# Optimization experiments

Measured on AMD Instinct MI355X. Metric: run time of the kernel, lower is better.

## Reference

```python
import jax, jax.numpy as jnp
import numpy as np

N_NODES = 50000
N_EDGES = 600000
N_GRAPHS = 64
IN_C, HID_C, OUT_C = 128, 128, 64


def gcn_conv(x, edge_index, W, b, num_nodes):
    """PyG GCNConv: x' = D^-1/2 (A + I) D^-1/2 (x W) + b, messages src->dst."""
    src, dst = edge_index[0], edge_index[1]
    # add self-loops
    loop = jnp.arange(num_nodes, dtype=src.dtype)
    src_full = jnp.concatenate([src, loop])
    dst_full = jnp.concatenate([dst, loop])
    # degree of A+I counted at the aggregation (dst) side
    deg = jax.ops.segment_sum(jnp.ones_like(dst_full, dtype=x.dtype), dst_full,
                              num_segments=num_nodes)
    dinv = jax.lax.rsqrt(jnp.maximum(deg, 1.0))
    norm = dinv[src_full] * dinv[dst_full]              # [E+N]
    h = x @ W                                           # [N, C_out] dense GEMM
    msg = h[src_full] * norm[:, None]                   # gather + scale
    out = jax.ops.segment_sum(msg, dst_full, num_segments=num_nodes)  # scatter-add
    return out + b


def global_mean_pool(x, batch, num_graphs):
    s = jax.ops.segment_sum(x, batch, num_segments=num_graphs)
    cnt = jax.ops.segment_sum(jnp.ones_like(batch, dtype=x.dtype), batch,
                              num_segments=num_graphs)
    return s / jnp.maximum(cnt, 1.0)[:, None]


def setup_inputs() -> dict:
    key = jax.random.key(0)
    ks = jax.random.split(key, 8)
    x = jax.random.normal(ks[0], (N_NODES, IN_C), dtype=jnp.float32)
    edge_index = jax.random.randint(ks[1], (2, N_EDGES), 0, N_NODES, dtype=jnp.int64)
    batch = jnp.sort(jax.random.randint(ks[2], (N_NODES,), 0, N_GRAPHS, dtype=jnp.int64))
    # Glorot-style init like PyG defaults
    W1 = jax.random.normal(ks[3], (IN_C, HID_C), dtype=jnp.float32) * (1.0 / np.sqrt(IN_C))
    b1 = jnp.zeros((HID_C,), dtype=jnp.float32)
    W2 = jax.random.normal(ks[4], (HID_C, OUT_C), dtype=jnp.float32) * (1.0 / np.sqrt(HID_C))
    b2 = jnp.zeros((OUT_C,), dtype=jnp.float32)
    return {"x": x, "W1": W1, "b1": b1, "W2": W2, "b2": b2,
            "edge_index": edge_index, "batch": batch}


def reference(x, W1, b1, W2, b2, edge_index, batch):
    h = gcn_conv(x, edge_index, W1, b1, N_NODES)
    h = jax.nn.relu(h)
    h = gcn_conv(h, edge_index, W2, b2, N_NODES)
    return global_mean_pool(h, batch, N_GRAPHS)  # [N_GRAPHS, OUT_C]
```

## Files before the change

kernel.cpp:

```cpp
#include <hip/hip_runtime.h>

#define NN 50000
#define NE 600000
#define NG 64
#define SCAN_T 1024
#define SCAN_NB ((NN + SCAN_T - 1) / SCAN_T)
#define PSPLIT 16

typedef unsigned int uint_t;
typedef unsigned short ushort_t;
typedef __attribute__((ext_vector_type(8))) short bf16x8;
typedef __attribute__((ext_vector_type(4))) float f32x4;

__device__ __forceinline__ ushort_t f2bf(float x) {
    uint_t u = __builtin_bit_cast(uint_t, x);
    u = (u + 0x7FFFu + ((u >> 16) & 1u)) >> 16;
    return (ushort_t)u;
}
__device__ __forceinline__ float bf_lo(uint_t p) {
    uint_t v = p << 16; return __builtin_bit_cast(float, v);
}
__device__ __forceinline__ float bf_hi(uint_t p) {
    uint_t v = p & 0xFFFF0000u; return __builtin_bit_cast(float, v);
}

__global__ void k_zero_deg(int* __restrict__ deg) {
    int i = blockIdx.x * blockDim.x + threadIdx.x;
    if (i < NN) deg[i] = 0;
}

__global__ void k_hist(const int* __restrict__ dst, int* __restrict__ deg) {
    int e = blockIdx.x * blockDim.x + threadIdx.x;
    if (e < NE) atomicAdd(&deg[dst[e]], 1);
}

__global__ __launch_bounds__(SCAN_T) void k_scan1(const int* __restrict__ deg,
                                                  int* __restrict__ blockSums) {
    __shared__ int s[SCAN_T];
    int i = blockIdx.x * SCAN_T + threadIdx.x;
    s[threadIdx.x] = (i < NN) ? deg[i] : 0;
    __syncthreads();
    for (int off = SCAN_T / 2; off > 0; off >>= 1) {
        if (threadIdx.x < off) s[threadIdx.x] += s[threadIdx.x + off];
        __syncthreads();
    }
    if (threadIdx.x == 0) blockSums[blockIdx.x] = s[0];
}

__global__ void k_scan2(const int* __restrict__ blockSums, int* __restrict__ blockOffs) {
    int t = threadIdx.x;
    int orig = (t < SCAN_NB) ? blockSums[t] : 0;
    int v = orig;
    for (int off = 1; off < 64; off <<= 1) {
        int u = __shfl_up(v, off);
        if (t >= off) v += u;
    }
    if (t < SCAN_NB) blockOffs[t] = v - orig;
}

__global__ __launch_bounds__(SCAN_T) void k_scan3(const int* __restrict__ deg,
                                                  const int* __restrict__ blockOffs,
                                                  int* __restrict__ rowptr,
                                                  int* __restrict__ cursor,
                                                  float* __restrict__ dinv) {
    __shared__ int s[SCAN_T];
    const int t = threadIdx.x;
    const int i = blockIdx.x * SCAN_T + t;
    const int v = (i < NN) ? deg[i] : 0;
    s[t] = v;
    __syncthreads();
    for (int off = 1; off < SCAN_T; off <<= 1) {
        int u = (t >= off) ? s[t - off] : 0;
        int cur = s[t];
        __syncthreads();
        s[t] = cur + u;
        __syncthreads();
    }
    if (i < NN) {
        int ex = blockOffs[blockIdx.x] + s[t] - v;
        rowptr[i] = ex;
        cursor[i] = ex;
        dinv[i] = rsqrtf((float)(v + 1));
    }
    if (i == 0) rowptr[NN] = NE;
}

__global__ void k_scatter(const int* __restrict__ src, const int* __restrict__ dst,
                          int* __restrict__ cursor, int* __restrict__ csr_src) {
    int e = blockIdx.x * blockDim.x + threadIdx.x;
    if (e >= NE) return;
    int d = dst[e];
    int p = atomicAdd(&cursor[d], 1);
    csr_src[p] = src[e];
}

__global__ void k_wprep(const float* __restrict__ W, ushort_t* __restrict__ Wt) {
    int idx = blockIdx.x * 256 + threadIdx.x;
    if (idx >= 128 * 128) return;
    int k = idx >> 7, n = idx & 127;
    Wt[n * 128 + k] = f2bf(W[idx]);
}

__global__ __launch_bounds__(256) void k_gemm_mfma(const float* __restrict__ X,
                                                   const ushort_t* __restrict__ Wt,
                                                   const float* __restrict__ dinv,
                                                   ushort_t* __restrict__ Hb) {
    __shared__ ushort_t xs[128 * 128];
    __shared__ ushort_t ws[128 * 128];
    const int tid = threadIdx.x;
    const int row0 = blockIdx.x * 128;

    for (int idx = tid; idx < 128 * 32; idx += 256) {
        int r = idx >> 5, c4 = idx & 31;
        int row = row0 + r;
        float4 v = make_float4(0.f, 0.f, 0.f, 0.f);
        if (row < NN) v = ((const float4*)X)[(long)row * 32 + c4];
        ushort4 o;
        o.x = f2bf(v.x); o.y = f2bf(v.y); o.z = f2bf(v.z); o.w = f2bf(v.w);
        uint_t byte = (uint_t)(r * 256 + c4 * 8) ^ (uint_t)((r & 7) << 4);
        *(ushort4*)((char*)xs + byte) = o;
    }
    for (int idx = tid; idx < 128 * 16; idx += 256) {
        int n = idx >> 4, c16 = idx & 15;
        uint4 v = ((const uint4*)Wt)[idx];
        uint_t byte = (uint_t)(n * 256 + c16 * 16) ^ (uint_t)((n & 7) << 4);
        *(uint4*)((char*)ws + byte) = v;
    }
    __syncthreads();

    const int w = tid >> 6;
    const int l = tid & 63;
    const int m0 = (w >> 1) * 4;
    const int n0 = (w & 1) * 4;
    const int lr = l & 15;
    const int kg = l >> 4;

    f32x4 acc[4][4] = {};
    for (int kk = 0; kk < 4; ++kk) {
        const int kb = kk * 64 + kg * 16;
        bf16x8 a[4], b[4];
#pragma unroll
        for (int m = 0; m < 4; ++m) {
            int r = (m0 + m) * 16 + lr;
            uint_t byte = (uint_t)(r * 256 + kb) ^ (uint_t)((r & 7) << 4);
            a[m] = *(const bf16x8*)((const char*)xs + byte);
        }
#pragma unroll
        for (int n = 0; n < 4; ++n) {
            int r = (n0 + n) * 16 + lr;
            uint_t byte = (uint_t)(r * 256 + kb) ^ (uint_t)((r & 7) << 4);
            b[n] = *(const bf16x8*)((const char*)ws + byte);
        }
#pragma unroll
        for (int m = 0; m < 4; ++m)
#pragma unroll
            for (int n = 0; n < 4; ++n)
                acc[m][n] = __builtin_amdgcn_mfma_f32_16x16x32_bf16(a[m], b[n], acc[m][n], 0, 0, 0);
    }

#pragma unroll
    for (int m = 0; m < 4; ++m) {
#pragma unroll
        for (int r = 0; r < 4; ++r) {
            int row = row0 + (m0 + m) * 16 + kg * 4 + r;
            if (row < NN) {
                float sc = dinv[row];
#pragma unroll
                for (int n = 0; n < 4; ++n) {
                    int col = (n0 + n) * 16 + lr;
                    Hb[(long)row * 128 + col] = f2bf(acc[m][n][r] * sc);
                }
            }
        }
    }
}

template <int C, int EPI>
__global__ __launch_bounds__(256) void k_agg(const int* __restrict__ rowptr,
                                             const int* __restrict__ csr_src,
                                             const float* __restrict__ dinv,
                                             const ushort_t* __restrict__ Hb,
                                             const float* __restrict__ bias,
                                             void* __restrict__ OUT) {
    constexpr int TPN = C / 8;
    constexpr int NPB = 256 / TPN;
    const int node = blockIdx.x * NPB + threadIdx.x / TPN;
    if (node >= NN) return;
    const int lane = threadIdx.x % TPN;
    const float dd = dinv[node];
    const uint4* __restrict__ H4 = (const uint4*)Hb;

    float a0, a1, a2, a3, a4, a5, a6, a7;
    {
        uint4 sv = H4[(long)node * TPN + lane];
        a0 = bf_lo(sv.x); a1 = bf_hi(sv.x);
        a2 = bf_lo(sv.y); a3 = bf_hi(sv.y);
        a4 = bf_lo(sv.z); a5 = bf_hi(sv.z);
        a6 = bf_lo(sv.w); a7 = bf_hi(sv.w);
    }

    const int beg = rowptr[node], end = rowptr[node + 1];
    int k = beg;
    const int n4 = beg + ((end - beg) & ~3);
    for (; k < n4; k += 4) {
        int s0 = csr_src[k + 0];
        int s1 = csr_src[k + 1];
        int s2 = csr_src[k + 2];
        int s3 = csr_src[k + 3];
        uint4 h0 = H4[(long)s0 * TPN + lane];
        uint4 h1 = H4[(long)s1 * TPN + lane];
        uint4 h2 = H4[(long)s2 * TPN + lane];
        uint4 h3 = H4[(long)s3 * TPN + lane];
        a0 += (bf_lo(h0.x) + bf_lo(h1.x)) + (bf_lo(h2.x) + bf_lo(h3.x));
        a1 += (bf_hi(h0.x) + bf_hi(h1.x)) + (bf_hi(h2.x) + bf_hi(h3.x));
        a2 += (bf_lo(h0.y) + bf_lo(h1.y)) + (bf_lo(h2.y) + bf_lo(h3.y));
        a3 += (bf_hi(h0.y) + bf_hi(h1.y)) + (bf_hi(h2.y) + bf_hi(h3.y));
        a4 += (bf_lo(h0.z) + bf_lo(h1.z)) + (bf_lo(h2.z) + bf_lo(h3.z));
        a5 += (bf_hi(h0.z) + bf_hi(h1.z)) + (bf_hi(h2.z) + bf_hi(h3.z));
        a6 += (bf_lo(h0.w) + bf_lo(h1.w)) + (bf_lo(h2.w) + bf_lo(h3.w));
        a7 += (bf_hi(h0.w) + bf_hi(h1.w)) + (bf_hi(h2.w) + bf_hi(h3.w));
    }
    for (; k < end; ++k) {
        int s = csr_src[k];
        uint4 h = H4[(long)s * TPN + lane];
        a0 += bf_lo(h.x); a1 += bf_hi(h.x);
        a2 += bf_lo(h.y); a3 += bf_hi(h.y);
        a4 += bf_lo(h.z); a5 += bf_hi(h.z);
        a6 += bf_lo(h.w); a7 += bf_hi(h.w);
    }

    a0 *= dd; a1 *= dd; a2 *= dd; a3 *= dd;
    a4 *= dd; a5 *= dd; a6 *= dd; a7 *= dd;

    if (EPI == 0) {
        const float4 b0 = *(const float4*)&bias[lane * 8];
        const float4 b1 = *(const float4*)&bias[lane * 8 + 4];
        a0 = fmaxf(a0 + b0.x, 0.f) * dd; a1 = fmaxf(a1 + b0.y, 0.f) * dd;
        a2 = fmaxf(a2 + b0.z, 0.f) * dd; a3 = fmaxf(a3 + b0.w, 0.f) * dd;
        a4 = fmaxf(a4 + b1.x, 0.f) * dd; a5 = fmaxf(a5 + b1.y, 0.f) * dd;
        a6 = fmaxf(a6 + b1.z, 0.f) * dd; a7 = fmaxf(a7 + b1.w, 0.f) * dd;
    }
    uint4 o;
    o.x = (uint_t)f2bf(a0) | ((uint_t)f2bf(a1) << 16);
    o.y = (uint_t)f2bf(a2) | ((uint_t)f2bf(a3) << 16);
    o.z = (uint_t)f2bf(a4) | ((uint_t)f2bf(a5) << 16);
    o.w = (uint_t)f2bf(a6) | ((uint_t)f2bf(a7) << 16);
    ((uint4*)OUT)[(long)node * TPN + lane] = o;
}

__global__ __launch_bounds__(256) void k_pool1(const ushort_t* __restrict__ V,
                                               const int* __restrict__ batch,
                                               float* __restrict__ partial) {
    const int g = blockIdx.x / PSPLIT;
    const int s = blockIdx.x % PSPLIT;
    int beg, end;
    {
        int lo = 0, hi = NN;
        while (lo < hi) { int mid = (lo + hi) >> 1; if (batch[mid] < g) lo = mid + 1; else hi = mid; }
        beg = lo;
        lo = beg; hi = NN;
        while (lo < hi) { int mid = (lo + hi) >> 1; if (batch[mid] < g + 1) lo = mid + 1; else hi = mid; }
        end = lo;
    }
    const int c = threadIdx.x & 31;
    const int rg = threadIdx.x >> 5;
    const uint2* __restrict__ V2 = (const uint2*)V;

    float4 acc = make_float4(0.f, 0.f, 0.f, 0.f);
    for (int n = beg + s * 8 + rg; n < end; n += PSPLIT * 8) {
        uint2 h = V2[(long)n * 32 + c];
        acc.x += bf_lo(h.x); acc.y += bf_hi(h.x);
        acc.z += bf_lo(h.y); acc.w += bf_hi(h.y);
    }
    __shared__ float4 red[8][33];
    red[rg][c] = acc;
    __syncthreads();
    if (rg == 0) {
        float4 t = red[0][c];
#pragma unroll
        for (int i = 1; i < 8; ++i) {
            float4 u = red[i][c];
            t.x += u.x; t.y += u.y; t.z += u.z; t.w += u.w;
        }
        ((float4*)partial)[(long)blockIdx.x * 32 + c] = t;
    }
}

__global__ __launch_bounds__(128) void k_pool2gemm(const float* __restrict__ partial,
                                                   const int* __restrict__ batch,
                                                   const float* __restrict__ W2,
                                                   const float* __restrict__ b2,
                                                   float* __restrict__ out) {
    const int g = blockIdx.x;
    const int t = threadIdx.x;
    int beg, end;
    {
        int lo = 0, hi = NN;
        while (lo < hi) { int mid = (lo + hi) >> 1; if (batch[mid] < g) lo = mid + 1; else hi = mid; }
        beg = lo;
        lo = beg; hi = NN;
        while (lo < hi) { int mid = (lo + hi) >> 1; if (batch[mid] < g + 1) lo = mid + 1; else hi = mid; }
        end = lo;
    }
    const int cnt = end - beg;
    __shared__ float P[128];
    float s = 0.f;
    for (int i = 0; i < PSPLIT; ++i) s += partial[(long)(g * PSPLIT + i) * 128 + t];
    P[t] = (cnt > 0) ? s / (float)cnt : 0.f;
    __syncthreads();
    if (t < 64) {
        float acc = 0.f;
        for (int k = 0; k < 128; ++k) acc += P[k] * W2[k * 64 + t];
        out[g * 64 + t] = (cnt > 0) ? acc + b2[t] : 0.f;
    }
}

extern "C" void kernel_launch(void* const* d_in, const int* in_sizes, int n_in,
                              void* d_out, int out_size, void* d_ws, size_t ws_size,
                              hipStream_t stream) {
    const float* x  = (const float*)d_in[0];
    const float* W1 = (const float*)d_in[1];
    const float* b1 = (const float*)d_in[2];
    const float* W2 = (const float*)d_in[3];
    const float* b2 = (const float*)d_in[4];
    const int* ei   = (const int*)d_in[5];
    const int* src  = ei;
    const int* dst  = ei + NE;
    const int* batch = (const int*)d_in[6];
    float* out = (float*)d_out;

    char* p = (char*)d_ws;
    int* deg       = (int*)p;          p += (size_t)NN * 4;
    int* rowptr    = (int*)p;          p += (size_t)(NN + 4) * 4;
    int* cursor    = (int*)p;          p += (size_t)NN * 4;
    int* csr_src   = (int*)p;          p += (size_t)NE * 4;
    int* blockSums = (int*)p;          p += (size_t)64 * 4;
    int* blockOffs = (int*)p;          p += (size_t)64 * 4;
    float* dinv    = (float*)p;        p += (size_t)NN * 4;
    float* partial = (float*)p;        p += (size_t)NG * PSPLIT * 128 * 4;
    ushort_t* Wt   = (ushort_t*)p;     p += (size_t)128 * 128 * 2;
    ushort_t* Hb   = (ushort_t*)p;     p += (size_t)NN * 128 * 2;
    ushort_t* H1b  = (ushort_t*)p;     p += (size_t)NN * 128 * 2;
    ushort_t* Vb   = (ushort_t*)p;     p += (size_t)NN * 128 * 2;

    k_wprep<<<64, 256, 0, stream>>>(W1, Wt);
    k_zero_deg<<<(NN + 255) / 256, 256, 0, stream>>>(deg);
    k_hist<<<(NE + 255) / 256, 256, 0, stream>>>(dst, deg);
    k_scan1<<<SCAN_NB, SCAN_T, 0, stream>>>(deg, blockSums);
    k_scan2<<<1, 64, 0, stream>>>(blockSums, blockOffs);
    k_scan3<<<SCAN_NB, SCAN_T, 0, stream>>>(deg, blockOffs, rowptr, cursor, dinv);
    k_scatter<<<(NE + 255) / 256, 256, 0, stream>>>(src, dst, cursor, csr_src);

    k_gemm_mfma<<<(NN + 127) / 128, 256, 0, stream>>>(x, Wt, dinv, Hb);
    k_agg<128, 0><<<(NN + 15) / 16, 256, 0, stream>>>(rowptr, csr_src, dinv, Hb, b1, H1b);

    k_agg<128, 1><<<(NN + 15) / 16, 256, 0, stream>>>(rowptr, csr_src, dinv, H1b, b1 , Vb);

    k_pool1<<<NG * PSPLIT, 256, 0, stream>>>(Vb, batch, partial);
    k_pool2gemm<<<NG, 128, 0, stream>>>(partial, batch, W2, b2, out);
}
```

Before: 168.0 us.

## Apply second-layer weight before aggregation to shrink gather width to 64

Restores the order GEMM-then-aggregate for layer 2. A new MFMA kernel multiplies the layer-1 output by W2 (scaled by dinv) into a 64-channel buffer, so the second gather/scatter pass and the pooling move 64 channels instead of 128. It also merges the tiny block-offset scan into the third scan kernel, removing one launch. The cost is an extra GEMM launch plus writing and reading the intermediate buffer, in exchange for halving the traffic of the edge-bound aggregation.

Measured after the change: 159.1 us. -5.3%, faster.

```diff
diff --git a/kernel.cpp b/kernel.cpp
--- a/kernel.cpp
+++ b/kernel.cpp
@@ -32,6 +32,19 @@
 __global__ void k_hist(const int* __restrict__ dst, int* __restrict__ deg) {
     int e = blockIdx.x * blockDim.x + threadIdx.x;
     if (e < NE) atomicAdd(&deg[dst[e]], 1);
+}
+
+__global__ void k_wprep(const float* __restrict__ W1, const float* __restrict__ W2,
+                        ushort_t* __restrict__ W1t, ushort_t* __restrict__ W2t) {
+    int idx = blockIdx.x * 256 + threadIdx.x;
+    if (idx < 128 * 128) {
+        int k = idx >> 7, n = idx & 127;
+        W1t[n * 128 + k] = f2bf(W1[idx]);
+    } else if (idx < 128 * 128 + 128 * 64) {
+        int j = idx - 128 * 128;
+        int k = j >> 6, n = j & 63;
+        W2t[n * 128 + k] = f2bf(W2[j]);
+    }
 }
 
 __global__ __launch_bounds__(SCAN_T) void k_scan1(const int* __restrict__ deg,
@@ -47,24 +60,23 @@
     if (threadIdx.x == 0) blockSums[blockIdx.x] = s[0];
 }
 
-__global__ void k_scan2(const int* __restrict__ blockSums, int* __restrict__ blockOffs) {
-    int t = threadIdx.x;
-    int orig = (t < SCAN_NB) ? blockSums[t] : 0;
-    int v = orig;
-    for (int off = 1; off < 64; off <<= 1) {
-        int u = __shfl_up(v, off);
-        if (t >= off) v += u;
-    }
-    if (t < SCAN_NB) blockOffs[t] = v - orig;
-}
-
 __global__ __launch_bounds__(SCAN_T) void k_scan3(const int* __restrict__ deg,
-                                                  const int* __restrict__ blockOffs,
+                                                  const int* __restrict__ blockSums,
                                                   int* __restrict__ rowptr,
                                                   int* __restrict__ cursor,
                                                   float* __restrict__ dinv) {
+    __shared__ int offs[64];
     __shared__ int s[SCAN_T];
     const int t = threadIdx.x;
+    if (t < 64) {
+        int orig = (t < SCAN_NB) ? blockSums[t] : 0;
+        int v = orig;
+        for (int off = 1; off < 64; off <<= 1) {
+            int u = __shfl_up(v, off);
+            if (t >= off) v += u;
+        }
+        offs[t] = v - orig;
+    }
     const int i = blockIdx.x * SCAN_T + t;
     const int v = (i < NN) ? deg[i] : 0;
     s[t] = v;
@@ -77,7 +89,7 @@
         __syncthreads();
     }
     if (i < NN) {
-        int ex = blockOffs[blockIdx.x] + s[t] - v;
+        int ex = offs[blockIdx.x] + s[t] - v;
         rowptr[i] = ex;
         cursor[i] = ex;
         dinv[i] = rsqrtf((float)(v + 1));
@@ -92,13 +104,6 @@
     int d = dst[e];
     int p = atomicAdd(&cursor[d], 1);
     csr_src[p] = src[e];
-}
-
-__global__ void k_wprep(const float* __restrict__ W, ushort_t* __restrict__ Wt) {
-    int idx = blockIdx.x * 256 + threadIdx.x;
-    if (idx >= 128 * 128) return;
-    int k = idx >> 7, n = idx & 127;
-    Wt[n * 128 + k] = f2bf(W[idx]);
 }
 
 __global__ __launch_bounds__(256) void k_gemm_mfma(const float* __restrict__ X,
@@ -175,13 +180,84 @@
     }
 }
 
+__global__ __launch_bounds__(256) void k_gemm_mfma2(const ushort_t* __restrict__ H1,
+                                                    const ushort_t* __restrict__ W2t,
+                                                    const float* __restrict__ dinv,
+                                                    ushort_t* __restrict__ G) {
+    __shared__ ushort_t xs[128 * 128];
+    __shared__ ushort_t ws2[64 * 128];
+    const int tid = threadIdx.x;
+    const int row0 = blockIdx.x * 128;
+
+    for (int idx = tid; idx < 128 * 16; idx += 256) {
+        int r = idx >> 4, c16 = idx & 15;
+        int row = row0 + r;
+        uint4 v = make_uint4(0u, 0u, 0u, 0u);
+        if (row < NN) v = ((const uint4*)H1)[(long)row * 16 + c16];
+        uint_t byte = (uint_t)(r * 256 + c16 * 16) ^ (uint_t)((r & 7) << 4);
+        *(uint4*)((char*)xs + byte) = v;
+    }
+    for (int idx = tid; idx < 64 * 16; idx += 256) {
+        int n = idx >> 4, c16 = idx & 15;
+        uint4 v = ((const uint4*)W2t)[idx];
+        uint_t byte = (uint_t)(n * 256 + c16 * 16) ^ (uint_t)((n & 7) << 4);
+        *(uint4*)((char*)ws2 + byte) = v;
+    }
+    __syncthreads();
+
+    const int w = tid >> 6;
+    const int l = tid & 63;
+    const int lr = l & 15;
+    const int kg = l >> 4;
+    const int m0 = w * 2;
+
+    f32x4 acc[2][4] = {};
+    for (int kk = 0; kk < 4; ++kk) {
+        const int kb = kk * 64 + kg * 16;
+        bf16x8 a[2], b[4];
+#pragma unroll
+        for (int m = 0; m < 2; ++m) {
+            int r = (m0 + m) * 16 + lr;
+            uint_t byte = (uint_t)(r * 256 + kb) ^ (uint_t)((r & 7) << 4);
+            a[m] = *(const bf16x8*)((const char*)xs + byte);
+        }
+#pragma unroll
+        for (int n = 0; n < 4; ++n) {
+            int r = n * 16 + lr;
+            uint_t byte = (uint_t)(r * 256 + kb) ^ (uint_t)((r & 7) << 4);
+            b[n] = *(const bf16x8*)((const char*)ws2 + byte);
+        }
+#pragma unroll
+        for (int m = 0; m < 2; ++m)
+#pragma unroll
+            for (int n = 0; n < 4; ++n)
+                acc[m][n] = __builtin_amdgcn_mfma_f32_16x16x32_bf16(a[m], b[n], acc[m][n], 0, 0, 0);
+    }
+
+#pragma unroll
+    for (int m = 0; m < 2; ++m) {
+#pragma unroll
+        for (int r = 0; r < 4; ++r) {
+            int row = row0 + (m0 + m) * 16 + kg * 4 + r;
+            if (row < NN) {
+                float sc = dinv[row];
+#pragma unroll
+                for (int n = 0; n < 4; ++n) {
+                    int col = n * 16 + lr;
+                    G[(long)row * 64 + col] = f2bf(acc[m][n][r] * sc);
+                }
+            }
+        }
+    }
+}
+
 template <int C, int EPI>
 __global__ __launch_bounds__(256) void k_agg(const int* __restrict__ rowptr,
                                              const int* __restrict__ csr_src,
                                              const float* __restrict__ dinv,
                                              const ushort_t* __restrict__ Hb,
                                              const float* __restrict__ bias,
-                                             void* __restrict__ OUT) {
+                                             ushort_t* __restrict__ OUT) {
     constexpr int TPN = C / 8;
     constexpr int NPB = 256 / TPN;
     const int node = blockIdx.x * NPB + threadIdx.x / TPN;
@@ -235,10 +311,10 @@
     if (EPI == 0) {
         const float4 b0 = *(const float4*)&bias[lane * 8];
         const float4 b1 = *(const float4*)&bias[lane * 8 + 4];
-        a0 = fmaxf(a0 + b0.x, 0.f) * dd; a1 = fmaxf(a1 + b0.y, 0.f) * dd;
-        a2 = fmaxf(a2 + b0.z, 0.f) * dd; a3 = fmaxf(a3 + b0.w, 0.f) * dd;
-        a4 = fmaxf(a4 + b1.x, 0.f) * dd; a5 = fmaxf(a5 + b1.y, 0.f) * dd;
-        a6 = fmaxf(a6 + b1.z, 0.f) * dd; a7 = fmaxf(a7 + b1.w, 0.f) * dd;
+        a0 = fmaxf(a0 + b0.x, 0.f); a1 = fmaxf(a1 + b0.y, 0.f);
+        a2 = fmaxf(a2 + b0.z, 0.f); a3 = fmaxf(a3 + b0.w, 0.f);
+        a4 = fmaxf(a4 + b1.x, 0.f); a5 = fmaxf(a5 + b1.y, 0.f);
+        a6 = fmaxf(a6 + b1.z, 0.f); a7 = fmaxf(a7 + b1.w, 0.f);
     }
     uint4 o;
     o.x = (uint_t)f2bf(a0) | ((uint_t)f2bf(a1) << 16);
@@ -262,37 +338,36 @@
         while (lo < hi) { int mid = (lo + hi) >> 1; if (batch[mid] < g + 1) lo = mid + 1; else hi = mid; }
         end = lo;
     }
-    const int c = threadIdx.x & 31;
-    const int rg = threadIdx.x >> 5;
+    const int c = threadIdx.x & 15;
+    const int rg = threadIdx.x >> 4;
     const uint2* __restrict__ V2 = (const uint2*)V;
 
     float4 acc = make_float4(0.f, 0.f, 0.f, 0.f);
-    for (int n = beg + s * 8 + rg; n < end; n += PSPLIT * 8) {
-        uint2 h = V2[(long)n * 32 + c];
+    for (int n = beg + s * 16 + rg; n < end; n += PSPLIT * 16) {
+        uint2 h = V2[(long)n * 16 + c];
         acc.x += bf_lo(h.x); acc.y += bf_hi(h.x);
         acc.z += bf_lo(h.y); acc.w += bf_hi(h.y);
     }
-    __shared__ float4 red[8][33];
+    __shared__ float4 red[16][17];
     red[rg][c] = acc;
     __syncthreads();
     if (rg == 0) {
         float4 t = red[0][c];
 #pragma unroll
-        for (int i = 1; i < 8; ++i) {
+        for (int i = 1; i < 16; ++i) {
             float4 u = red[i][c];
             t.x += u.x; t.y += u.y; t.z += u.z; t.w += u.w;
         }
-        ((float4*)partial)[(long)blockIdx.x * 32 + c] = t;
-    }
-}
-
-__global__ __launch_bounds__(128) void k_pool2gemm(const float* __restrict__ partial,
-                                                   const int* __restrict__ batch,
-                                                   const float* __restrict__ W2,
-                                                   const float* __restrict__ b2,
-                                                   float* __restrict__ out) {
+        ((float4*)partial)[(long)blockIdx.x * 16 + c] = t;
+    }
+}
+
+__global__ __launch_bounds__(64) void k_pool2(const float* __restrict__ partial,
+                                              const int* __restrict__ batch,
+                                              const float* __restrict__ b2,
+                                              float* __restrict__ out) {
     const int g = blockIdx.x;
-    const int t = threadIdx.x;
+    const int ch = threadIdx.x;
     int beg, end;
     {
         int lo = 0, hi = NN;
@@ -302,17 +377,10 @@
         while (lo < hi) { int mid = (lo + hi) >> 1; if (batch[mid] < g + 1) lo = mid + 1; else hi = mid; }
         end = lo;
     }
-    const int cnt = end - beg;
-    __shared__ float P[128];
     float s = 0.f;
-    for (int i = 0; i < PSPLIT; ++i) s += partial[(long)(g * PSPLIT + i) * 128 + t];
-    P[t] = (cnt > 0) ? s / (float)cnt : 0.f;
-    __syncthreads();
-    if (t < 64) {
-        float acc = 0.f;
-        for (int k = 0; k < 128; ++k) acc += P[k] * W2[k * 64 + t];
-        out[g * 64 + t] = (cnt > 0) ? acc + b2[t] : 0.f;
-    }
+    for (int i = 0; i < PSPLIT; ++i) s += partial[(long)(g * PSPLIT + i) * 64 + ch];
+    int cnt = end - beg;
+    out[g * 64 + ch] = (cnt > 0) ? (s / (float)cnt + b2[ch]) : 0.f;
 }
 
 extern "C" void kernel_launch(void* const* d_in, const int* in_sizes, int n_in,
@@ -335,27 +403,28 @@
     int* cursor    = (int*)p;          p += (size_t)NN * 4;
     int* csr_src   = (int*)p;          p += (size_t)NE * 4;
     int* blockSums = (int*)p;          p += (size_t)64 * 4;
-    int* blockOffs = (int*)p;          p += (size_t)64 * 4;
     float* dinv    = (float*)p;        p += (size_t)NN * 4;
-    float* partial = (float*)p;        p += (size_t)NG * PSPLIT * 128 * 4;
-    ushort_t* Wt   = (ushort_t*)p;     p += (size_t)128 * 128 * 2;
+    float* partial = (float*)p;        p += (size_t)NG * PSPLIT * 64 * 4;
+    ushort_t* W1t  = (ushort_t*)p;     p += (size_t)128 * 128 * 2;
+    ushort_t* W2t  = (ushort_t*)p;     p += (size_t)64 * 128 * 2;
     ushort_t* Hb   = (ushort_t*)p;     p += (size_t)NN * 128 * 2;
     ushort_t* H1b  = (ushort_t*)p;     p += (size_t)NN * 128 * 2;
-    ushort_t* Vb   = (ushort_t*)p;     p += (size_t)NN * 128 * 2;
-
-    k_wprep<<<64, 256, 0, stream>>>(W1, Wt);
+    ushort_t* Gb   = (ushort_t*)p;     p += (size_t)NN * 64 * 2;
+    ushort_t* Vb   = (ushort_t*)p;     p += (size_t)NN * 64 * 2;
+
+    k_wprep<<<96, 256, 0, stream>>>(W1, W2, W1t, W2t);
     k_zero_deg<<<(NN + 255) / 256, 256, 0, stream>>>(deg);
     k_hist<<<(NE + 255) / 256, 256, 0, stream>>>(dst, deg);
     k_scan1<<<SCAN_NB, SCAN_T, 0, stream>>>(deg, blockSums);
-    k_scan2<<<1, 64, 0, stream>>>(blockSums, blockOffs);
-    k_scan3<<<SCAN_NB, SCAN_T, 0, stream>>>(deg, blockOffs, rowptr, cursor, dinv);
+    k_scan3<<<SCAN_NB, SCAN_T, 0, stream>>>(deg, blockSums, rowptr, cursor, dinv);
     k_scatter<<<(NE + 255) / 256, 256, 0, stream>>>(src, dst, cursor, csr_src);
 
-    k_gemm_mfma<<<(NN + 127) / 128, 256, 0, stream>>>(x, Wt, dinv, Hb);
+    k_gemm_mfma<<<(NN + 127) / 128, 256, 0, stream>>>(x, W1t, dinv, Hb);
     k_agg<128, 0><<<(NN + 15) / 16, 256, 0, stream>>>(rowptr, csr_src, dinv, Hb, b1, H1b);
 
-    k_agg<128, 1><<<(NN + 15) / 16, 256, 0, stream>>>(rowptr, csr_src, dinv, H1b, b1 , Vb);
+    k_gemm_mfma2<<<(NN + 127) / 128, 256, 0, stream>>>(H1b, W2t, dinv, Gb);
+    k_agg<64, 1><<<(NN + 31) / 32, 256, 0, stream>>>(rowptr, csr_src, dinv, Gb, b1 , Vb);
 
     k_pool1<<<NG * PSPLIT, 256, 0, stream>>>(Vb, batch, partial);
-    k_pool2gemm<<<NG, 128, 0, stream>>>(partial, batch, W2, b2, out);
-}
+    k_pool2<<<NG, 64, 0, stream>>>(partial, batch, b2, out);
+}
```
